# Optimization experiments

Hardware: AMD Instinct MI355X
Metric: run time of the kernel (lower is better)

Reference implementation:

```python
import jax, jax.numpy as jnp
import numpy as np

H = 16
D_MODEL = 1024
D_K = D_MODEL // H


def setup_inputs() -> dict:
    key = jax.random.key(0)
    ks = jax.random.split(key, 12)
    B, S = 2, 2048
    scale = 1.0 / np.sqrt(D_MODEL)
    inp = {
        "query": jax.random.normal(ks[0], (B, S, D_MODEL), jnp.float32),
        "key": jax.random.normal(ks[1], (B, S, D_MODEL), jnp.float32),
        "value": jax.random.normal(ks[2], (B, S, D_MODEL), jnp.float32),
        "mask": jnp.ones((B, 1, S), jnp.int32),
        "Wq": jax.random.normal(ks[3], (D_MODEL, D_MODEL), jnp.float32) * scale,
        "bq": jnp.zeros((D_MODEL,), jnp.float32),
        "Wk": jax.random.normal(ks[4], (D_MODEL, D_MODEL), jnp.float32) * scale,
        "bk": jnp.zeros((D_MODEL,), jnp.float32),
        "Wv": jax.random.normal(ks[5], (D_MODEL, D_MODEL), jnp.float32) * scale,
        "bv": jnp.zeros((D_MODEL,), jnp.float32),
        "Wo": jax.random.normal(ks[6], (D_MODEL, D_MODEL), jnp.float32) * scale,
        "bo": jnp.zeros((D_MODEL,), jnp.float32),
    }
    return inp


def reference(query, key, value, mask, Wq, bq, Wk, bk, Wv, bv, Wo, bo):
    B, S, _ = query.shape
    # QKV projections, split heads: [B, S, D] -> [B, H, S, d_k]
    def proj(x, W, b):
        y = x @ W.T + b
        return y.reshape(B, -1, H, D_K).transpose(0, 2, 1, 3)

    q = proj(query, Wq, bq)
    k = proj(key, Wk, bk)
    v = proj(value, Wv, bv)

    # scaled dot-product attention with full score matrix [B, H, Sq, Sk]
    scores = jnp.einsum("bhqd,bhkd->bhqk", q, k) / np.sqrt(D_K)
    m = mask[:, None, :, :]  # unsqueeze head dim: [B, 1, 1_or_S, S]
    scores = jnp.where(m == 0, jnp.float32(-1e9), scores)
    p_attn = jax.nn.softmax(scores, axis=-1)  # dropout p=0.0 (eval)
    x = jnp.einsum("bhqk,bhkd->bhqd", p_attn, v)

    # merge heads and output projection
    x = x.transpose(0, 2, 1, 3).reshape(B, -1, H * D_K)
    return x @ Wo.T + bo
```

## Files before the change

### kernel.cpp

```cpp
#include <hip/hip_runtime.h>
#include <hip/hip_bf16.h>
#include <stdint.h>

typedef unsigned short us;
typedef __bf16 bf8 __attribute__((ext_vector_type(8)));
typedef float  f4  __attribute__((ext_vector_type(4)));

typedef unsigned int __attribute__((address_space(1))) as1_uint;
typedef unsigned int __attribute__((address_space(3))) as3_uint;

__device__ __forceinline__ void async_ld16(const void* g, void* l) {
    __builtin_amdgcn_global_load_lds((as1_uint*)g, (as3_uint*)l, 16, 0, 0);
}

__device__ __forceinline__ us f2bf(float f) {
    __hip_bfloat16 h = __float2bfloat16(f);
    us u;
    __builtin_memcpy(&u, &h, 2);
    return u;
}

__device__ __forceinline__ float fexp2(float x) {
#if __has_builtin(__builtin_amdgcn_exp2f)
    return __builtin_amdgcn_exp2f(x);
#else
    return exp2f(x);
#endif
}

#define SCALE_Q 0.18033688011112042f

__global__ __launch_bounds__(256)
void convert_all(const float* __restrict__ s0, const float* __restrict__ s1,
                 const float* __restrict__ s2, const float* __restrict__ s3,
                 const float* __restrict__ s4, const float* __restrict__ s5,
                 const float* __restrict__ s6,
                 us* __restrict__ d0, us* __restrict__ d1, us* __restrict__ d2,
                 us* __restrict__ d3, us* __restrict__ d4, us* __restrict__ d5,
                 us* __restrict__ d6)
{
    size_t i4 = (((size_t)blockIdx.x * 256) + threadIdx.x) << 2;
    const float* src; us* dst; size_t off;
    if (i4 < ((size_t)3 << 22)) {
        unsigned seg = (unsigned)(i4 >> 22);
        off = i4 & (((size_t)1 << 22) - 1);
        src = seg == 0 ? s0 : (seg == 1 ? s1 : s2);
        dst = seg == 0 ? d0 : (seg == 1 ? d1 : d2);
    } else {
        size_t j = i4 - ((size_t)3 << 22);
        unsigned seg = (unsigned)(j >> 20);
        off = j & (((size_t)1 << 20) - 1);
        src = seg == 0 ? s3 : (seg == 1 ? s4 : (seg == 2 ? s5 : s6));
        dst = seg == 0 ? d3 : (seg == 1 ? d4 : (seg == 2 ? d5 : d6));
    }
    float4 f = *(const float4*)(src + off);
    ushort4 o;
    o.x = f2bf(f.x); o.y = f2bf(f.y); o.z = f2bf(f.z); o.w = f2bf(f.w);
    *(ushort4*)(dst + off) = o;
}

template<int MODE, int BN>
__device__ __forceinline__
void gemm_body(const us* __restrict__ A, const us* __restrict__ W,
               const float* __restrict__ bias, void* __restrict__ out,
               float scale, int bx, int by)
{
    __shared__ us lA[128 * 32];
    __shared__ us lB[BN * 32];

    const int tid  = threadIdx.x;
    const int wv   = tid >> 6;
    const int lane = tid & 63;
    const int l15  = lane & 15;
    const int quad = lane >> 4;
    const int kq   = quad << 3;
    const int cr   = quad << 2;
    const int srow = lane >> 2;
    const int scol = (lane & 3) << 3;
    const int m0   = by << 7;
    const int n0   = bx * BN;
    constexpr int MJ = (BN == 128) ? 4 : 2;
    const int wm = (BN == 128) ? ((wv >> 1) << 6) : (wv << 5);
    const int wn = (BN == 128) ? ((wv & 1) << 6) : 0;

    f4 acc[4][MJ];
    const f4 zero = {0.f, 0.f, 0.f, 0.f};
#pragma unroll
    for (int i = 0; i < 4; ++i)
#pragma unroll
        for (int j = 0; j < MJ; ++j) acc[i][j] = zero;

    for (int kt = 0; kt < 1024; kt += 32) {
#pragma unroll
        for (int s = 0; s < 2; ++s) {
            const int chunk = wv * 2 + s;
            const int row   = chunk * 16 + srow;
            async_ld16(A + (size_t)(m0 + row) * 1024 + kt + scol, &lA[chunk * 512]);
        }
        if (BN == 128) {
#pragma unroll
            for (int s = 0; s < 2; ++s) {
                const int chunk = wv * 2 + s;
                const int row   = chunk * 16 + srow;
                async_ld16(W + (size_t)(n0 + row) * 1024 + kt + scol, &lB[chunk * 512]);
            }
        } else {
            const int row = wv * 16 + srow;
            async_ld16(W + (size_t)(n0 + row) * 1024 + kt + scol, &lB[wv * 512]);
        }
        __syncthreads();

        bf8 wf[4], xf[MJ];
#pragma unroll
        for (int i = 0; i < 4; ++i)
            wf[i] = *(const bf8*)&lB[(wn + i * 16 + l15) * 32 + kq];
#pragma unroll
        for (int j = 0; j < MJ; ++j)
            xf[j] = *(const bf8*)&lA[(wm + j * 16 + l15) * 32 + kq];
#pragma unroll
        for (int i = 0; i < 4; ++i)
#pragma unroll
            for (int j = 0; j < MJ; ++j)
                acc[i][j] = __builtin_amdgcn_mfma_f32_16x16x32_bf16(wf[i], xf[j], acc[i][j], 0, 0, 0);
        __syncthreads();
    }

    if (MODE == 2) {
        us* o = (us*)out;
#pragma unroll
        for (int j = 0; j < MJ; ++j) {
            const int f = m0 + wm + j * 16 + l15;
            const float bf_ = bias[f];
            const int hh = f >> 6, dd = f & 63;
#pragma unroll
            for (int i = 0; i < 4; ++i) {
                const int tokb = n0 + wn + i * 16 + cr;
                const int bb = tokb >> 11, ss = tokb & 2047;
                us hp[4];
#pragma unroll
                for (int r = 0; r < 4; ++r) hp[r] = f2bf(acc[i][j][r] + bf_);
                uint2 w;
                w.x = (unsigned)hp[0] | ((unsigned)hp[1] << 16);
                w.y = (unsigned)hp[2] | ((unsigned)hp[3] << 16);
                *(uint2*)&o[((size_t)((bb * 16 + hh) * 64 + dd) << 11) + ss] = w;
            }
        }
        return;
    }

#pragma unroll
    for (int i = 0; i < 4; ++i) {
        const int gnb = n0 + wn + i * 16 + cr;
        const f4 bj = *(const f4*)&bias[gnb];
        if (MODE == 0) {
            us* o = (us*)out;
            const int hh = gnb >> 6, dd = gnb & 63;
#pragma unroll
            for (int j = 0; j < MJ; ++j) {
                const int gm = m0 + wm + j * 16 + l15;
                const int bb = gm >> 11, ss = gm & 2047;
                us hp[4];
#pragma unroll
                for (int r = 0; r < 4; ++r)
                    hp[r] = f2bf((acc[i][j][r] + bj[r]) * scale);
                uint2 w;
                w.x = (unsigned)hp[0] | ((unsigned)hp[1] << 16);
                w.y = (unsigned)hp[2] | ((unsigned)hp[3] << 16);
                *(uint2*)&o[(((size_t)(bb * 16 + hh) * 2048 + ss) << 6) + dd] = w;
            }
        } else {
            float* o = (float*)out;
#pragma unroll
            for (int j = 0; j < MJ; ++j) {
                const int gm = m0 + wm + j * 16 + l15;
                f4 v;
#pragma unroll
                for (int r = 0; r < 4; ++r) v[r] = acc[i][j][r] + bj[r];
                *(f4*)&o[((size_t)gm << 10) + gnb] = v;
            }
        }
    }
}

__global__ __launch_bounds__(256)
void gemm_qkv(const us* __restrict__ XQ, const us* __restrict__ XK,
              const us* __restrict__ XV,
              const us* __restrict__ WQ, const us* __restrict__ WK,
              const us* __restrict__ WV,
              const float* __restrict__ bq, const float* __restrict__ bk,
              const float* __restrict__ bv,
              us* __restrict__ QP, us* __restrict__ KP, us* __restrict__ VT)
{
    const int z = blockIdx.z;
    if (z == 2) {
        gemm_body<2, 128>(WV, XV, bv, VT, 1.0f, blockIdx.y, blockIdx.x);
        return;
    }
    const us* A = z == 0 ? XQ : XK;
    const us* W = z == 0 ? WQ : WK;
    const float* b = z == 0 ? bq : bk;
    us* o = z == 0 ? QP : KP;
    const float scale = z == 0 ? SCALE_Q : 1.0f;
    gemm_body<0, 128>(A, W, b, o, scale, blockIdx.x, blockIdx.y);
}

__global__ __launch_bounds__(256)
void gemm_o(const us* __restrict__ A, const us* __restrict__ W,
            const float* __restrict__ bias, float* __restrict__ out)
{
    gemm_body<1, 64>(A, W, bias, out, 1.0f, blockIdx.x, blockIdx.y);
}

__global__ __launch_bounds__(256)
void flash_attn(const us* __restrict__ Qp, const us* __restrict__ Kp,
                const us* __restrict__ Vtp, const int* __restrict__ maskp,
                us* __restrict__ ctx)
{
    __shared__ us lK[64 * 64];
    __shared__ us lVt[64 * 64];
    __shared__ us lP[4 * 32 * 72];
    __shared__ float lmask[64];

    const int tid  = threadIdx.x;
    const int wv   = tid >> 6;
    const int lane = tid & 63;
    const int l15  = lane & 15;
    const int quad = lane >> 4;
    const int cr   = quad << 2;
    const int l7   = l15 & 7;

    const int q0 = blockIdx.x << 7;
    const int h  = blockIdx.y;
    const int b  = blockIdx.z;

    const size_t headoff = ((size_t)(b * 16 + h)) << 17;
    const us* Qh  = Qp  + headoff;
    const us* Kh  = Kp  + headoff;
    const us* Vth = Vtp + headoff;

    bf8 qf[2][2];
#pragma unroll
    for (int nt = 0; nt < 2; ++nt)
#pragma unroll
        for (int kb = 0; kb < 2; ++kb)
            qf[nt][kb] = *(const bf8*)(Qh + ((size_t)(q0 + wv * 32 + nt * 16 + l15) << 6)
                                          + kb * 32 + (quad << 3));

    const f4 zero = {0.f, 0.f, 0.f, 0.f};
    f4 of[4][2];
#pragma unroll
    for (int dt = 0; dt < 4; ++dt)
#pragma unroll
        for (int nt = 0; nt < 2; ++nt) of[dt][nt] = zero;
    float li[2] = {0.f, 0.f};

    us* lPw = lP + wv * (32 * 72);

    const int sr = tid >> 3;
    const int sc = tid & 7;

    for (int kt0 = 0; kt0 < 2048; kt0 += 64) {
        __syncthreads();

#pragma unroll
        for (int it = 0; it < 2; ++it) {
            const int r = sr + 32 * it;
            const int sw = (sc ^ (r & 7)) << 3;
            uint4 kv = *(const uint4*)(Kh + ((size_t)(kt0 + r) << 6) + sc * 8);
            *(uint4*)&lK[(r << 6) + sw] = kv;
            uint4 vv = *(const uint4*)(Vth + (size_t)r * 2048 + kt0 + sc * 8);
            *(uint4*)&lVt[(r << 6) + sw] = vv;
        }
        if (tid < 64)
            lmask[tid] = (maskp[((size_t)b << 11) + kt0 + tid] == 0) ? 0.0f : 1.0f;
        __syncthreads();

        float rs[2] = {0.f, 0.f};
#pragma unroll
        for (int kt = 0; kt < 4; ++kt) {
            const int krow = (kt * 16 + l15) << 6;
            bf8 kf0 = *(const bf8*)&lK[krow + ((quad ^ l7) << 3)];
            bf8 kf1 = *(const bf8*)&lK[krow + (((4 + quad) ^ l7) << 3)];
            f4 st[2];
#pragma unroll
            for (int nt = 0; nt < 2; ++nt) {
                st[nt] = __builtin_amdgcn_mfma_f32_16x16x32_bf16(kf0, qf[nt][0], zero, 0, 0, 0);
                st[nt] = __builtin_amdgcn_mfma_f32_16x16x32_bf16(kf1, qf[nt][1], st[nt], 0, 0, 0);
            }
            const f4 mr = *(const f4*)&lmask[kt * 16 + cr];
#pragma unroll
            for (int nt = 0; nt < 2; ++nt) {
                us hp[4];
#pragma unroll
                for (int r = 0; r < 4; ++r) {
                    const float p = fexp2(st[nt][r]) * mr[r];
                    rs[nt] += p;
                    hp[r] = f2bf(p);
                }
                uint2 w;
                w.x = (unsigned)hp[0] | ((unsigned)hp[1] << 16);
                w.y = (unsigned)hp[2] | ((unsigned)hp[3] << 16);
                *(uint2*)&lPw[(nt * 16 + l15) * 72 + kt * 16 + cr] = w;
            }
        }
#pragma unroll
        for (int nt = 0; nt < 2; ++nt) {
            float r2 = rs[nt];
            r2 += __shfl_xor(r2, 16, 64);
            r2 += __shfl_xor(r2, 32, 64);
            li[nt] += r2;
        }

#pragma unroll
        for (int kb = 0; kb < 2; ++kb) {
            bf8 pfr[2];
#pragma unroll
            for (int nt = 0; nt < 2; ++nt)
                pfr[nt] = *(const bf8*)&lPw[(nt * 16 + l15) * 72 + kb * 32 + (quad << 3)];
#pragma unroll
            for (int dt = 0; dt < 4; ++dt) {
                bf8 vf = *(const bf8*)&lVt[((dt * 16 + l15) << 6) + (((kb * 4 + quad) ^ l7) << 3)];
#pragma unroll
                for (int nt = 0; nt < 2; ++nt)
                    of[dt][nt] = __builtin_amdgcn_mfma_f32_16x16x32_bf16(vf, pfr[nt], of[dt][nt], 0, 0, 0);
            }
        }
    }

#pragma unroll
    for (int nt = 0; nt < 2; ++nt) {
        const float linv = 1.0f / li[nt];
        const int tok = q0 + wv * 32 + nt * 16 + l15;
        const size_t rowb = (((size_t)(b * 2048 + tok)) << 10) + (h << 6);
#pragma unroll
        for (int dt = 0; dt < 4; ++dt) {
            us hp[4];
#pragma unroll
            for (int r = 0; r < 4; ++r) hp[r] = f2bf(of[dt][nt][r] * linv);
            uint2 w;
            w.x = (unsigned)hp[0] | ((unsigned)hp[1] << 16);
            w.y = (unsigned)hp[2] | ((unsigned)hp[3] << 16);
            *(uint2*)&ctx[rowb + dt * 16 + cr] = w;
        }
    }
}

extern "C" void kernel_launch(void* const* d_in, const int* in_sizes, int n_in,
                              void* d_out, int out_size, void* d_ws, size_t ws_size,
                              hipStream_t stream)
{
    const float* q    = (const float*)d_in[0];
    const float* k    = (const float*)d_in[1];
    const float* v    = (const float*)d_in[2];
    const int*   mask = (const int*)d_in[3];
    const float* Wq   = (const float*)d_in[4];
    const float* bq   = (const float*)d_in[5];
    const float* Wk   = (const float*)d_in[6];
    const float* bk   = (const float*)d_in[7];
    const float* Wv   = (const float*)d_in[8];
    const float* bv   = (const float*)d_in[9];
    const float* Wo   = (const float*)d_in[10];
    const float* bo   = (const float*)d_in[11];
    float* out = (float*)d_out;

    us* ws  = (us*)d_ws;
    us* XQ  = ws;
    us* XK  = ws + 4194304;
    us* XV  = ws + 8388608;
    us* WQb = ws + 12582912;
    us* WKb = ws + 13631488;
    us* WVb = ws + 14680064;
    us* WOb = ws + 15728640;
    us* QP  = ws + 16777216;
    us* KP  = ws + 20971520;
    us* VT  = ws + 25165824;
    us* CTX = XQ;

    convert_all<<<16384, 256, 0, stream>>>(q, k, v, Wq, Wk, Wv, Wo,
                                           XQ, XK, XV, WQb, WKb, WVb, WOb);
    gemm_qkv<<<dim3(8, 32, 3), 256, 0, stream>>>(XQ, XK, XV, WQb, WKb, WVb,
                                                 bq, bk, bv, QP, KP, VT);
    flash_attn<<<dim3(16, 16, 2), 256, 0, stream>>>(QP, KP, VT, mask, CTX);
    gemm_o<<<dim3(16, 32), 256, 0, stream>>>(CTX, WOb, bo, out);
}
```

Measured before the change: 250.4 us.

## Double-buffer K/V tiles in flash attention with register prefetch

```diff
diff --git a/kernel.cpp b/kernel.cpp
--- a/kernel.cpp
+++ b/kernel.cpp
@@ -216,10 +216,10 @@
                 const us* __restrict__ Vtp, const int* __restrict__ maskp,
                 us* __restrict__ ctx)
 {
-    __shared__ us lK[64 * 64];
-    __shared__ us lVt[64 * 64];
+    __shared__ us lK[2][64 * 64];
+    __shared__ us lVt[2][64 * 64];
     __shared__ us lP[4 * 32 * 72];
-    __shared__ float lmask[64];
+    __shared__ float lmask[2][64];
 
     const int tid  = threadIdx.x;
     const int wv   = tid >> 6;
@@ -259,35 +259,56 @@
     const int sr = tid >> 3;
     const int sc = tid & 7;
 
-    for (int kt0 = 0; kt0 < 2048; kt0 += 64) {
-        __syncthreads();
-
-#pragma unroll
-        for (int it = 0; it < 2; ++it) {
-            const int r = sr + 32 * it;
-            const int sw = (sc ^ (r & 7)) << 3;
-            uint4 kv = *(const uint4*)(Kh + ((size_t)(kt0 + r) << 6) + sc * 8);
-            *(uint4*)&lK[(r << 6) + sw] = kv;
-            uint4 vv = *(const uint4*)(Vth + (size_t)r * 2048 + kt0 + sc * 8);
-            *(uint4*)&lVt[(r << 6) + sw] = vv;
-        }
-        if (tid < 64)
-            lmask[tid] = (maskp[((size_t)b << 11) + kt0 + tid] == 0) ? 0.0f : 1.0f;
-        __syncthreads();
+    uint4 rk[2], rv[2];
+    float rm = 1.0f;
+
+#define FA_ISSUE(kt0)                                                          \
+    {                                                                          \
+        _Pragma("unroll")                                                      \
+        for (int it = 0; it < 2; ++it) {                                       \
+            const int r = sr + 32 * it;                                        \
+            rk[it] = *(const uint4*)(Kh + ((size_t)((kt0) + r) << 6) + sc * 8);\
+            rv[it] = *(const uint4*)(Vth + (size_t)r * 2048 + (kt0) + sc * 8); \
+        }                                                                      \
+        if (tid < 64)                                                          \
+            rm = (maskp[((size_t)b << 11) + (kt0) + tid] == 0) ? 0.0f : 1.0f;  \
+    }
+
+#define FA_WRITE(bi)                                                           \
+    {                                                                          \
+        _Pragma("unroll")                                                      \
+        for (int it = 0; it < 2; ++it) {                                       \
+            const int r = sr + 32 * it;                                        \
+            const int sw = (sc ^ (r & 7)) << 3;                                \
+            *(uint4*)&lK[bi][(r << 6) + sw] = rk[it];                          \
+            *(uint4*)&lVt[bi][(r << 6) + sw] = rv[it];                         \
+        }                                                                      \
+        if (tid < 64) lmask[bi][tid] = rm;                                     \
+    }
+
+    FA_ISSUE(0);
+    FA_WRITE(0);
+    FA_ISSUE(64);
+    __syncthreads();
+
+    for (int t = 0; t < 32; ++t) {
+        const int cur = t & 1;
+        const us* lKc  = lK[cur];
+        const us* lVtc = lVt[cur];
 
         float rs[2] = {0.f, 0.f};
 #pragma unroll
         for (int kt = 0; kt < 4; ++kt) {
             const int krow = (kt * 16 + l15) << 6;
-            bf8 kf0 = *(const bf8*)&lK[krow + ((quad ^ l7) << 3)];
-            bf8 kf1 = *(const bf8*)&lK[krow + (((4 + quad) ^ l7) << 3)];
+            bf8 kf0 = *(const bf8*)&lKc[krow + ((quad ^ l7) << 3)];
+            bf8 kf1 = *(const bf8*)&lKc[krow + (((4 + quad) ^ l7) << 3)];
             f4 st[2];
 #pragma unroll
             for (int nt = 0; nt < 2; ++nt) {
                 st[nt] = __builtin_amdgcn_mfma_f32_16x16x32_bf16(kf0, qf[nt][0], zero, 0, 0, 0);
                 st[nt] = __builtin_amdgcn_mfma_f32_16x16x32_bf16(kf1, qf[nt][1], st[nt], 0, 0, 0);
             }
-            const f4 mr = *(const f4*)&lmask[kt * 16 + cr];
+            const f4 mr = *(const f4*)&lmask[cur][kt * 16 + cr];
 #pragma unroll
             for (int nt = 0; nt < 2; ++nt) {
                 us hp[4];
@@ -319,13 +340,22 @@
                 pfr[nt] = *(const bf8*)&lPw[(nt * 16 + l15) * 72 + kb * 32 + (quad << 3)];
 #pragma unroll
             for (int dt = 0; dt < 4; ++dt) {
-                bf8 vf = *(const bf8*)&lVt[((dt * 16 + l15) << 6) + (((kb * 4 + quad) ^ l7) << 3)];
+                bf8 vf = *(const bf8*)&lVtc[((dt * 16 + l15) << 6) + (((kb * 4 + quad) ^ l7) << 3)];
 #pragma unroll
                 for (int nt = 0; nt < 2; ++nt)
                     of[dt][nt] = __builtin_amdgcn_mfma_f32_16x16x32_bf16(vf, pfr[nt], of[dt][nt], 0, 0, 0);
             }
         }
-    }
+
+        if (t < 31) {
+            __syncthreads();
+            FA_WRITE(cur ^ 1);
+            if (t < 30) FA_ISSUE((t + 2) * 64);
+            __syncthreads();
+        }
+    }
+#undef FA_ISSUE
+#undef FA_WRITE
 
 #pragma unroll
     for (int nt = 0; nt < 2; ++nt) {
```

Result: slower. 278.1 us (+11.0%).
